# Kernel optimization log

Hardware: AMD Instinct MI355X
Metric: run time of the kernel (lower is better)

Reference implementation:

```python
import jax, jax.numpy as jnp
import numpy as np

NUM_ACTIVE = 2  # top-k active experts

def setup_inputs() -> dict:
    key = jax.random.key(0)
    ks = jax.random.split(key, 5)
    B, N, D, H, E = 8192, 16, 128, 384, 8
    x = jax.random.normal(ks[0], (B, N, D), dtype=jnp.float32)
    # xavier-ish scales for stability
    router_w = jax.random.normal(ks[1], (E, N * D), dtype=jnp.float32) * (1.0 / np.sqrt(N * D))
    w1 = jax.random.normal(ks[2], (E, N, D, H), dtype=jnp.float32) * (1.0 / np.sqrt(D))
    w_gate = jax.random.normal(ks[3], (E, N, D, H), dtype=jnp.float32) * (1.0 / np.sqrt(D))
    w2 = jax.random.normal(ks[4], (E, N, H, D), dtype=jnp.float32) * (1.0 / np.sqrt(H))
    return {"x": x, "router_w": router_w, "w1": w1, "w_gate": w_gate, "w2": w2}

def reference(x, router_w, w1, w_gate, w2):
    B, N, D = x.shape
    E = w1.shape[0]
    # shared router over flattened heads
    router_logits = x.reshape(B, N * D) @ router_w.T            # (B, E)
    topk_logits, topk_idx = jax.lax.top_k(router_logits, NUM_ACTIVE)
    topk_w = jax.nn.softmax(topk_logits, axis=-1)               # (B, K)
    # combined routing weight per (token, expert); zero if expert not selected
    onehot = jax.nn.one_hot(topk_idx, E, dtype=x.dtype)         # (B, K, E)
    w_tok_exp = jnp.einsum('bk,bke->be', topk_w, onehot)        # (B, E)
    out = jnp.zeros_like(x)
    # loop over fixed, small expert count; unselected tokens get weight 0
    for e in range(E):
        h1 = jnp.einsum('bnd,ndh->bnh', x, w1[e])
        gate = jnp.einsum('bnd,ndh->bnh', x, w_gate[e])
        h = h1 * jax.nn.silu(gate)                              # SwiGLU (dropout=0 / eval)
        out_e = jnp.einsum('bnh,nhd->bnd', h, w2[e])
        out = out + w_tok_exp[:, e][:, None, None] * out_e
    return out
```

## Files before the change

### kernel.cpp

```cpp
#include <hip/hip_runtime.h>

#define NTOK  8192
#define NHEAD 16
#define DDIM  128
#define HDIM  384
#define NEXP  8
#define TILE  128
#define ENTRIES 1280

typedef __attribute__((ext_vector_type(8))) short short8;
typedef __attribute__((ext_vector_type(4))) float f32x4;

#define SZ_WP    (128UL*12*24*512*2)
#define OFF_WP   0UL
#define OFF_ROUT (OFF_WP + SZ_WP)
#define OFF_CNT  (OFF_ROUT + 8192UL*16)
#define OFF_TAB  (OFF_CNT + 256)
#define OFF_LIST (OFF_TAB + 2UL*ENTRIES*16)
#define OFF_WL   (OFF_LIST + 2UL*8192*4)

struct Routing { int i0, i1; float w0, w1; };

__device__ __forceinline__ unsigned short f2bf(float f) {
  unsigned int u = __float_as_uint(f);
  u += 0x7fffu + ((u >> 16) & 1u);
  return (unsigned short)(u >> 16);
}

__device__ __forceinline__ void dma16(const unsigned short* g, char* l) {
  __builtin_amdgcn_global_load_lds(
      (const __attribute__((address_space(1))) unsigned int*)g,
      (__attribute__((address_space(3))) unsigned int*)l, 16, 0, 0);
}

__global__ __launch_bounds__(256) void convA_kernel(
    const float* __restrict__ w1, const float* __restrict__ wg,
    unsigned short* __restrict__ wP) {
  __shared__ float ls[32][388];
  const int kk = blockIdx.x;
  const int en = blockIdx.y;
  const int z  = blockIdx.z;
  const float* src = (z == 0 ? w1 : wg) + ((size_t)en * DDIM + kk * 32) * HDIM;
  const int tid = threadIdx.x;
  #pragma unroll
  for (int i = 0; i < 12; ++i) {
    int f4 = i * 256 + tid;
    int row = f4 / 96, c4 = f4 % 96;
    float4 v = reinterpret_cast<const float4*>(src + (size_t)row * HDIM)[c4];
    ls[row][c4*4+0] = v.x; ls[row][c4*4+1] = v.y;
    ls[row][c4*4+2] = v.z; ls[row][c4*4+3] = v.w;
  }
  __syncthreads();
  #pragma unroll
  for (int i = 0; i < 6; ++i) {
    int fid = i * 256 + tid;
    int ct = fid >> 6, lane = fid & 63;
    int r0 = (lane >> 4) * 8, c = ct * 16 + (lane & 15);
    unsigned short o[8];
    #pragma unroll
    for (int j = 0; j < 8; ++j) o[j] = f2bf(ls[r0 + j][c]);
    size_t off = (((size_t)en * 12 + (ct >> 1)) * 24 + (z * 8 + kk * 2 + (ct & 1))) * 512
               + (size_t)lane * 8;
    reinterpret_cast<uint4*>(wP + off)[0] =
        make_uint4((unsigned)o[0] | ((unsigned)o[1] << 16),
                   (unsigned)o[2] | ((unsigned)o[3] << 16),
                   (unsigned)o[4] | ((unsigned)o[5] << 16),
                   (unsigned)o[6] | ((unsigned)o[7] << 16));
  }
}

__global__ __launch_bounds__(256) void convB_kernel(
    const float* __restrict__ w2, unsigned short* __restrict__ wP) {
  __shared__ float ls[32][132];
  const int kk = blockIdx.x;
  const int en = blockIdx.y;
  const float* src = w2 + ((size_t)en * HDIM + kk * 32) * DDIM;
  const int tid = threadIdx.x;
  #pragma unroll
  for (int i = 0; i < 4; ++i) {
    int f4 = i * 256 + tid;
    int row = f4 >> 5, c4 = f4 & 31;
    float4 v = reinterpret_cast<const float4*>(src + (size_t)row * DDIM)[c4];
    ls[row][c4*4+0] = v.x; ls[row][c4*4+1] = v.y;
    ls[row][c4*4+2] = v.z; ls[row][c4*4+3] = v.w;
  }
  __syncthreads();
  #pragma unroll
  for (int i = 0; i < 2; ++i) {
    int fid = i * 256 + tid;
    int ct = fid >> 6, lane = fid & 63;
    int r0 = (lane >> 4) * 8, c = ct * 16 + (lane & 15);
    unsigned short o[8];
    #pragma unroll
    for (int j = 0; j < 8; ++j) o[j] = f2bf(ls[r0 + j][c]);
    size_t off = (((size_t)en * 12 + kk) * 24 + (16 + ct)) * 512 + (size_t)lane * 8;
    reinterpret_cast<uint4*>(wP + off)[0] =
        make_uint4((unsigned)o[0] | ((unsigned)o[1] << 16),
                   (unsigned)o[2] | ((unsigned)o[3] << 16),
                   (unsigned)o[4] | ((unsigned)o[5] << 16),
                   (unsigned)o[6] | ((unsigned)o[7] << 16));
  }
}

__global__ __launch_bounds__(256) void router_kernel(
    const float* __restrict__ x, const float* __restrict__ rw,
    Routing* __restrict__ routing) {
  const int lane = threadIdx.x & 63;
  const int wgid = blockIdx.x * 4 + (threadIdx.x >> 6);
  const int tok0 = wgid * 4;
  float acc[4][8];
  #pragma unroll
  for (int t = 0; t < 4; ++t)
    #pragma unroll
    for (int e = 0; e < 8; ++e) acc[t][e] = 0.f;
  const float4* xr = reinterpret_cast<const float4*>(x);
  const float4* wr = reinterpret_cast<const float4*>(rw);
  #pragma unroll
  for (int c = 0; c < 8; ++c) {
    float4 wv[8];
    #pragma unroll
    for (int e = 0; e < 8; ++e) wv[e] = wr[e * 512 + c * 64 + lane];
    #pragma unroll
    for (int t = 0; t < 4; ++t) {
      float4 xv = xr[(size_t)(tok0 + t) * 512 + c * 64 + lane];
      #pragma unroll
      for (int e = 0; e < 8; ++e)
        acc[t][e] += xv.x * wv[e].x + xv.y * wv[e].y + xv.z * wv[e].z + xv.w * wv[e].w;
    }
  }
  #pragma unroll
  for (int t = 0; t < 4; ++t)
    #pragma unroll
    for (int e = 0; e < 8; ++e) {
      acc[t][e] += __shfl_xor(acc[t][e], 1);
      acc[t][e] += __shfl_xor(acc[t][e], 2);
      acc[t][e] += __shfl_xor(acc[t][e], 4);
    }
  const int l3 = lane & 7;
  #pragma unroll
  for (int t = 0; t < 4; ++t) {
    float v0 = (l3 & 1) ? acc[t][1] : acc[t][0];
    float v1 = (l3 & 1) ? acc[t][3] : acc[t][2];
    float v2 = (l3 & 1) ? acc[t][5] : acc[t][4];
    float v3 = (l3 & 1) ? acc[t][7] : acc[t][6];
    float u0 = (l3 & 2) ? v1 : v0;
    float u1 = (l3 & 2) ? v3 : v2;
    float sel = (l3 & 4) ? u1 : u0;
    sel += __shfl_xor(sel, 8);
    sel += __shfl_xor(sel, 16);
    sel += __shfl_xor(sel, 32);
    float le[8];
    #pragma unroll
    for (int e = 0; e < 8; ++e) le[e] = __shfl(sel, e);
    if (lane == 0) {
      int tok = tok0 + t;
      int i0 = 0; float m0 = le[0];
      #pragma unroll
      for (int e = 1; e < 8; ++e) if (le[e] > m0) { m0 = le[e]; i0 = e; }
      int i1 = -1; float m1 = -3.4e38f;
      #pragma unroll
      for (int e = 0; e < 8; ++e) if (e != i0 && le[e] > m1) { m1 = le[e]; i1 = e; }
      float ed = __expf(m1 - m0);
      Routing r; r.i0 = i0; r.i1 = i1;
      r.w0 = 1.f / (1.f + ed); r.w1 = ed / (1.f + ed);
      routing[tok] = r;
    }
  }
}

__global__ __launch_bounds__(256) void count_kernel(
    const Routing* __restrict__ routing, int* __restrict__ cnt) {
  const int s = blockIdx.x >> 3, e = blockIdx.x & 7;
  const int tid = threadIdx.x;
  int c = 0;
  for (int t = tid; t < NTOK; t += 256) {
    Routing r = routing[t];
    c += ((s == 0 ? r.i0 : r.i1) == e);
  }
  c += __shfl_xor(c, 32); c += __shfl_xor(c, 16); c += __shfl_xor(c, 8);
  c += __shfl_xor(c, 4);  c += __shfl_xor(c, 2);  c += __shfl_xor(c, 1);
  __shared__ int wsum[4];
  if ((tid & 63) == 0) wsum[tid >> 6] = c;
  __syncthreads();
  if (tid == 0) cnt[blockIdx.x] = wsum[0] + wsum[1] + wsum[2] + wsum[3];
}

__global__ void build_kernel(const int* __restrict__ cnt, int* __restrict__ cur,
                             int4* __restrict__ table) {
  const int tid = threadIdx.x;
  for (int i = tid; i < 2 * ENTRIES; i += 256)
    table[i] = make_int4(0, 0, 0, 0);
  __syncthreads();
  if (tid < 16) {
    int s = tid >> 3, e = tid & 7;
    int base = 0;
    for (int k = 0; k < e; ++k) base += cnt[s * 8 + k];
    cur[tid] = base;
  }
  __syncthreads();
  if (tid < 16) {
    int s = tid >> 3, xcd = tid & 7;
    int j = 0;
    int base = 0;
    for (int e = 0; e < 8; ++e) {
      int c = cnt[s * 8 + e];
      #pragma unroll
      for (int nn = 0; nn < 2; ++nn) {
        int n = xcd + nn * 8;
        for (int t = 0; t < c; t += TILE) {
          int rc = c - t; if (rc > TILE) rc = TILE;
          table[s * ENTRIES + xcd + 8 * j] = make_int4(e, base + t, rc, n);
          ++j;
        }
      }
      base += c;
    }
  }
}

__global__ __launch_bounds__(256) void compact_kernel(
    const Routing* __restrict__ routing, const int* __restrict__ cur,
    int* __restrict__ list, float* __restrict__ wl) {
  const int s = blockIdx.x >> 3, e = blockIdx.x & 7;
  const int tid = threadIdx.x;
  __shared__ int ps[256];
  int myc = 0;
  for (int t = tid; t < NTOK; t += 256) {
    Routing r = routing[t];
    myc += ((s == 0 ? r.i0 : r.i1) == e);
  }
  ps[tid] = myc;
  __syncthreads();
  for (int off = 1; off < 256; off <<= 1) {
    int v = (tid >= off) ? ps[tid - off] : 0;
    __syncthreads();
    ps[tid] += v;
    __syncthreads();
  }
  int base = cur[blockIdx.x] + ps[tid] - myc;
  for (int t = tid; t < NTOK; t += 256) {
    Routing r = routing[t];
    int ei = (s == 0 ? r.i0 : r.i1);
    if (ei == e) {
      list[s * NTOK + base] = t;
      wl[s * NTOK + base] = (s == 0 ? r.w0 : r.w1);
      ++base;
    }
  }
}

__global__ __launch_bounds__(512, 4) void expert_kernel(
    const float* __restrict__ x,
    const unsigned short* __restrict__ wP,
    const int* __restrict__ list, const float* __restrict__ wl,
    const int4* __restrict__ table,
    float* __restrict__ out, const int slot)
{
  extern __shared__ char smem[];
  char* wb  = smem;
  char* pwb = smem + 49152;
  const int4 tb = table[slot * ENTRIES + blockIdx.x];
  const int e = tb.x, rbeg = tb.y, rcnt = tb.z, n = tb.w;
  if (rcnt == 0) return;
  const int* lst = list + slot * NTOK + rbeg;
  const float* wls = wl + slot * NTOK + rbeg;
  const int tid = threadIdx.x;
  const int wid = tid >> 6, lane = tid & 63;
  const int lr = lane & 15, lq = lane >> 4;
  const int tq = wid >> 1, ch = wid & 1;
  char* pq = pwb + tq * 2304;
  const f32x4 z4 = {0.f, 0.f, 0.f, 0.f};

  const unsigned short* wsrc = wP + (size_t)(e * NHEAD + n) * (12 * 24 * 512);

  short8 a[2][4];
  #pragma unroll
  for (int mi = 0; mi < 2; ++mi) {
    int row = tq * 32 + mi * 16 + lr;
    int ok = (row < rcnt);
    int tok = ok ? lst[row] : 0;
    const float* xp = x + ((size_t)tok * NHEAD + n) * DDIM;
    #pragma unroll
    for (int kk = 0; kk < 4; ++kk) {
      const float4* q = reinterpret_cast<const float4*>(xp + kk * 32 + lq * 8);
      float4 v0 = q[0], v1 = q[1];
      if (!ok) { v0 = make_float4(0,0,0,0); v1 = make_float4(0,0,0,0); }
      short8 t;
      t[0] = (short)f2bf(v0.x); t[1] = (short)f2bf(v0.y);
      t[2] = (short)f2bf(v0.z); t[3] = (short)f2bf(v0.w);
      t[4] = (short)f2bf(v1.x); t[5] = (short)f2bf(v1.y);
      t[6] = (short)f2bf(v1.z); t[7] = (short)f2bf(v1.w);
      a[mi][kk] = t;
    }
  }

  f32x4 acc[2][4];
  #pragma unroll
  for (int mi = 0; mi < 2; ++mi)
    #pragma unroll
    for (int ct = 0; ct < 4; ++ct) acc[mi][ct] = z4;

  #pragma unroll
  for (int i = 0; i < 3; ++i) {
    int seg = wid * 3 + i;
    dma16(wsrc + (size_t)seg * 512 + lane * 8, wb + seg * 1024);
  }

  #pragma unroll
  for (int c = 0; c < 12; ++c) {
    const int p = c & 1;
    char* wbp = wb + p * 24576;

    asm volatile("s_waitcnt lgkmcnt(0)" ::: "memory");
    __builtin_amdgcn_s_barrier();
    __builtin_amdgcn_sched_barrier(0);

    if (c < 11) {
      char* wbn = wb + (p ^ 1) * 24576;
      #pragma unroll
      for (int i = 0; i < 3; ++i) {
        int seg = wid * 3 + i;
        dma16(wsrc + ((size_t)(c + 1) * 24 + seg) * 512 + lane * 8, wbn + seg * 1024);
      }
      asm volatile("s_waitcnt vmcnt(3)" ::: "memory");
    } else {
      asm volatile("s_waitcnt vmcnt(0)" ::: "memory");
    }
    __builtin_amdgcn_s_barrier();
    __builtin_amdgcn_sched_barrier(0);

    {
      f32x4 ah[2], ag[2];
      ah[0] = ah[1] = z4; ag[0] = ag[1] = z4;
      #pragma unroll
      for (int kk = 0; kk < 4; ++kk) {
        short8 b1 = *reinterpret_cast<const short8*>(wbp + (kk * 2 + ch) * 1024 + lane * 16);
        short8 bg = *reinterpret_cast<const short8*>(wbp + 8192 + (kk * 2 + ch) * 1024 + lane * 16);
        #pragma unroll
        for (int mi = 0; mi < 2; ++mi) {
          ah[mi] = __builtin_amdgcn_mfma_f32_16x16x32_bf16(a[mi][kk], b1, ah[mi], 0, 0, 0);
          ag[mi] = __builtin_amdgcn_mfma_f32_16x16x32_bf16(a[mi][kk], bg, ag[mi], 0, 0, 0);
        }
      }
      #pragma unroll
      for (int mi = 0; mi < 2; ++mi)
        #pragma unroll
        for (int r = 0; r < 4; ++r) {
          float h1 = ah[mi][r], g = ag[mi][r];
          float val = h1 * g * __builtin_amdgcn_rcpf(1.f + __expf(-g));
          int rowq = mi * 16 + lq * 4 + r;
          int h = ch * 16 + lr;
          *reinterpret_cast<unsigned short*>(pq + rowq * 72 + h * 2) = f2bf(val);
        }
    }

    asm volatile("s_waitcnt lgkmcnt(0)" ::: "memory");
    __builtin_amdgcn_s_barrier();
    __builtin_amdgcn_sched_barrier(0);

    {
      short8 a2[2];
      #pragma unroll
      for (int mi = 0; mi < 2; ++mi)
        a2[mi] = *reinterpret_cast<const short8*>(pq + (mi * 16 + lr) * 72 + lq * 16);
      #pragma unroll
      for (int ct = 0; ct < 4; ++ct) {
        short8 b = *reinterpret_cast<const short8*>(wbp + (16 + ch * 4 + ct) * 1024 + lane * 16);
        acc[0][ct] = __builtin_amdgcn_mfma_f32_16x16x32_bf16(a2[0], b, acc[0][ct], 0, 0, 0);
        acc[1][ct] = __builtin_amdgcn_mfma_f32_16x16x32_bf16(a2[1], b, acc[1][ct], 0, 0, 0);
      }
    }
  }

  #pragma unroll
  for (int mi = 0; mi < 2; ++mi)
    #pragma unroll
    for (int r = 0; r < 4; ++r) {
      int row = tq * 32 + mi * 16 + lq * 4 + r;
      if (row < rcnt) {
        int tok = lst[row];
        float wt = wls[row];
        float* op = out + ((size_t)tok * NHEAD + n) * DDIM;
        #pragma unroll
        for (int ct = 0; ct < 4; ++ct) {
          int col = (ch * 4 + ct) * 16 + lr;
          float v = acc[mi][ct][r] * wt;
          if (slot == 0) op[col] = v;
          else          op[col] += v;
        }
      }
    }
}

extern "C" void kernel_launch(void* const* d_in, const int* in_sizes, int n_in,
                              void* d_out, int out_size, void* d_ws, size_t ws_size,
                              hipStream_t stream) {
  const float* x  = (const float*)d_in[0];
  const float* rw = (const float*)d_in[1];
  const float* w1 = (const float*)d_in[2];
  const float* wg = (const float*)d_in[3];
  const float* w2 = (const float*)d_in[4];
  float* out = (float*)d_out;
  char* ws = (char*)d_ws;

  unsigned short* wP = (unsigned short*)(ws + OFF_WP);
  Routing* routing = (Routing*)(ws + OFF_ROUT);
  int* cnt = (int*)(ws + OFF_CNT);
  int* cur = cnt + 16;
  int4* table = (int4*)(ws + OFF_TAB);
  int* list = (int*)(ws + OFF_LIST);
  float* wl = (float*)(ws + OFF_WL);

  convA_kernel<<<dim3(4, 128, 2), 256, 0, stream>>>(w1, wg, wP);
  convB_kernel<<<dim3(12, 128, 1), 256, 0, stream>>>(w2, wP);
  router_kernel<<<512, 256, 0, stream>>>(x, rw, routing);
  count_kernel<<<16, 256, 0, stream>>>(routing, cnt);
  build_kernel<<<1, 256, 0, stream>>>(cnt, cur, table);
  compact_kernel<<<16, 256, 0, stream>>>(routing, cur, list, wl);
  expert_kernel<<<ENTRIES, 512, 58368, stream>>>(
      x, wP, list, wl, table, out, 0);
  expert_kernel<<<ENTRIES, 512, 58368, stream>>>(
      x, wP, list, wl, table, out, 1);
}
```

Before: 274.0 us.

## Keep expert weights in registers and stream pre-gathered bf16 token tiles

```diff
diff --git a/kernel.cpp b/kernel.cpp
--- a/kernel.cpp
+++ b/kernel.cpp
@@ -5,8 +5,6 @@
 #define DDIM  128
 #define HDIM  384
 #define NEXP  8
-#define TILE  128
-#define ENTRIES 1280
 
 typedef __attribute__((ext_vector_type(8))) short short8;
 typedef __attribute__((ext_vector_type(4))) float f32x4;
@@ -15,9 +13,11 @@
 #define OFF_WP   0UL
 #define OFF_ROUT (OFF_WP + SZ_WP)
 #define OFF_CNT  (OFF_ROUT + 8192UL*16)
-#define OFF_TAB  (OFF_CNT + 256)
-#define OFF_LIST (OFF_TAB + 2UL*ENTRIES*16)
+#define OFF_LIST (OFF_CNT + 256)
 #define OFF_WL   (OFF_LIST + 2UL*8192*4)
+#define OFF_XG   (OFF_WL + 2UL*8192*4)
+#define XG_SLOT  (16UL*8192*128*2)
+#define XG_PAD   32768UL
 
 struct Routing { int i0, i1; float w0, w1; };
 
@@ -185,36 +185,13 @@
   if (tid == 0) cnt[blockIdx.x] = wsum[0] + wsum[1] + wsum[2] + wsum[3];
 }
 
-__global__ void build_kernel(const int* __restrict__ cnt, int* __restrict__ cur,
-                             int4* __restrict__ table) {
-  const int tid = threadIdx.x;
-  for (int i = tid; i < 2 * ENTRIES; i += 256)
-    table[i] = make_int4(0, 0, 0, 0);
-  __syncthreads();
+__global__ void build_kernel(const int* __restrict__ cnt, int* __restrict__ cur) {
+  int tid = threadIdx.x;
   if (tid < 16) {
     int s = tid >> 3, e = tid & 7;
-    int base = 0;
-    for (int k = 0; k < e; ++k) base += cnt[s * 8 + k];
-    cur[tid] = base;
-  }
-  __syncthreads();
-  if (tid < 16) {
-    int s = tid >> 3, xcd = tid & 7;
-    int j = 0;
-    int base = 0;
-    for (int e = 0; e < 8; ++e) {
-      int c = cnt[s * 8 + e];
-      #pragma unroll
-      for (int nn = 0; nn < 2; ++nn) {
-        int n = xcd + nn * 8;
-        for (int t = 0; t < c; t += TILE) {
-          int rc = c - t; if (rc > TILE) rc = TILE;
-          table[s * ENTRIES + xcd + 8 * j] = make_int4(e, base + t, rc, n);
-          ++j;
-        }
-      }
-      base += c;
-    }
+    int b = 0;
+    for (int k = 0; k < e; ++k) b += cnt[s * 8 + k];
+    cur[tid] = b;
   }
 }
 
@@ -249,147 +226,136 @@
   }
 }
 
-__global__ __launch_bounds__(512, 4) void expert_kernel(
-    const float* __restrict__ x,
+__global__ __launch_bounds__(256) void gather_kernel(
+    const float* __restrict__ x, const int* __restrict__ list,
+    unsigned short* __restrict__ xg, const int slot) {
+  const int tid = threadIdx.x;
+  const int n = tid >> 4, j = tid & 15;
+  for (int it = 0; it < 64; ++it) {
+    int pos = blockIdx.x * 64 + it;
+    int t = list[slot * NTOK + pos];
+    const float* src = x + ((size_t)t * NHEAD + n) * DDIM + j * 8;
+    float4 v0 = reinterpret_cast<const float4*>(src)[0];
+    float4 v1 = reinterpret_cast<const float4*>(src)[1];
+    uint4 w = make_uint4(
+        (unsigned)f2bf(v0.x) | ((unsigned)f2bf(v0.y) << 16),
+        (unsigned)f2bf(v0.z) | ((unsigned)f2bf(v0.w) << 16),
+        (unsigned)f2bf(v1.x) | ((unsigned)f2bf(v1.y) << 16),
+        (unsigned)f2bf(v1.z) | ((unsigned)f2bf(v1.w) << 16));
+    *reinterpret_cast<uint4*>(xg + ((size_t)n * NTOK + pos) * 128 + (size_t)((j ^ (pos & 7)) * 8)) = w;
+  }
+}
+
+__global__ __launch_bounds__(512, 2) void expert_kernel(
+    const unsigned short* __restrict__ xg,
     const unsigned short* __restrict__ wP,
     const int* __restrict__ list, const float* __restrict__ wl,
-    const int4* __restrict__ table,
+    const int* __restrict__ cnt,
     float* __restrict__ out, const int slot)
 {
   extern __shared__ char smem[];
-  char* wb  = smem;
-  char* pwb = smem + 49152;
-  const int4 tb = table[slot * ENTRIES + blockIdx.x];
-  const int e = tb.x, rbeg = tb.y, rcnt = tb.z, n = tb.w;
-  if (rcnt == 0) return;
-  const int* lst = list + slot * NTOK + rbeg;
-  const float* wls = wl + slot * NTOK + rbeg;
+  char* xls = smem;
+  char* P   = smem + 32768;
+  const int bid = blockIdx.x;
+  const int e = bid >> 5, n = (bid >> 1) & 15, kpar = bid & 1;
+  const int cntE  = cnt[slot * 8 + e];
+  const int ebase = cnt[16 + slot * 8 + e];
+  const int ntiles = (cntE + 127) >> 7;
+  if (kpar >= ntiles) return;
   const int tid = threadIdx.x;
   const int wid = tid >> 6, lane = tid & 63;
   const int lr = lane & 15, lq = lane >> 4;
-  const int tq = wid >> 1, ch = wid & 1;
-  char* pq = pwb + tq * 2304;
   const f32x4 z4 = {0.f, 0.f, 0.f, 0.f};
 
   const unsigned short* wsrc = wP + (size_t)(e * NHEAD + n) * (12 * 24 * 512);
-
-  short8 a[2][4];
-  #pragma unroll
-  for (int mi = 0; mi < 2; ++mi) {
-    int row = tq * 32 + mi * 16 + lr;
-    int ok = (row < rcnt);
-    int tok = ok ? lst[row] : 0;
-    const float* xp = x + ((size_t)tok * NHEAD + n) * DDIM;
+  short8 w1r[3][4], wgr[3][4], w2r[12];
+  #pragma unroll
+  for (int c = 0; c < 3; ++c) {
+    const int ctg = wid * 3 + c;
     #pragma unroll
     for (int kk = 0; kk < 4; ++kk) {
-      const float4* q = reinterpret_cast<const float4*>(xp + kk * 32 + lq * 8);
-      float4 v0 = q[0], v1 = q[1];
-      if (!ok) { v0 = make_float4(0,0,0,0); v1 = make_float4(0,0,0,0); }
-      short8 t;
-      t[0] = (short)f2bf(v0.x); t[1] = (short)f2bf(v0.y);
-      t[2] = (short)f2bf(v0.z); t[3] = (short)f2bf(v0.w);
-      t[4] = (short)f2bf(v1.x); t[5] = (short)f2bf(v1.y);
-      t[6] = (short)f2bf(v1.z); t[7] = (short)f2bf(v1.w);
-      a[mi][kk] = t;
-    }
-  }
-
-  f32x4 acc[2][4];
-  #pragma unroll
-  for (int mi = 0; mi < 2; ++mi)
-    #pragma unroll
-    for (int ct = 0; ct < 4; ++ct) acc[mi][ct] = z4;
-
-  #pragma unroll
-  for (int i = 0; i < 3; ++i) {
-    int seg = wid * 3 + i;
-    dma16(wsrc + (size_t)seg * 512 + lane * 8, wb + seg * 1024);
-  }
-
-  #pragma unroll
-  for (int c = 0; c < 12; ++c) {
-    const int p = c & 1;
-    char* wbp = wb + p * 24576;
-
+      size_t off = ((size_t)(ctg >> 1) * 24 + (kk * 2 + (ctg & 1))) * 512 + (size_t)lane * 8;
+      w1r[c][kk] = *reinterpret_cast<const short8*>(wsrc + off);
+      wgr[c][kk] = *reinterpret_cast<const short8*>(wsrc + off + 8 * 512);
+    }
+  }
+  #pragma unroll
+  for (int kk = 0; kk < 12; ++kk)
+    w2r[kk] = *reinterpret_cast<const short8*>(
+        wsrc + ((size_t)kk * 24 + 16 + wid) * 512 + (size_t)lane * 8);
+
+  const unsigned short* xbase = xg + ((size_t)n * NTOK + ebase) * 128;
+
+  {
+    const unsigned short* src = xbase + (size_t)kpar * 128 * 128 + wid * 2048;
+    #pragma unroll
+    for (int i = 0; i < 4; ++i)
+      dma16(src + i * 512 + lane * 8, xls + wid * 4096 + i * 1024);
+  }
+  asm volatile("s_waitcnt vmcnt(0)" ::: "memory");
+  __builtin_amdgcn_s_barrier();
+
+  for (int t = kpar; t < ntiles; t += 2) {
+    #pragma unroll 2
+    for (int mi = 0; mi < 8; ++mi) {
+      const int row = mi * 16 + lr;
+      const int key = ((ebase + row) & 7) << 4;
+      short8 a[4];
+      #pragma unroll
+      for (int kk = 0; kk < 4; ++kk)
+        a[kk] = *reinterpret_cast<const short8*>(xls + row * 256 + ((kk * 64 + lq * 16) ^ key));
+      #pragma unroll
+      for (int c = 0; c < 3; ++c) {
+        f32x4 ah = z4, ag = z4;
+        #pragma unroll
+        for (int kk = 0; kk < 4; ++kk) {
+          ah = __builtin_amdgcn_mfma_f32_16x16x32_bf16(a[kk], w1r[c][kk], ah, 0, 0, 0);
+          ag = __builtin_amdgcn_mfma_f32_16x16x32_bf16(a[kk], wgr[c][kk], ag, 0, 0, 0);
+        }
+        const int pcol = (wid * 3 + c) * 16 + lr;
+        #pragma unroll
+        for (int r = 0; r < 4; ++r) {
+          float h1 = ah[r], g = ag[r];
+          float val = h1 * g * __builtin_amdgcn_rcpf(1.f + __expf(-g));
+          int prow = mi * 16 + lq * 4 + r;
+          *reinterpret_cast<unsigned short*>(P + prow * 772 + pcol * 2) = f2bf(val);
+        }
+      }
+    }
     asm volatile("s_waitcnt lgkmcnt(0)" ::: "memory");
     __builtin_amdgcn_s_barrier();
-    __builtin_amdgcn_sched_barrier(0);
-
-    if (c < 11) {
-      char* wbn = wb + (p ^ 1) * 24576;
-      #pragma unroll
-      for (int i = 0; i < 3; ++i) {
-        int seg = wid * 3 + i;
-        dma16(wsrc + ((size_t)(c + 1) * 24 + seg) * 512 + lane * 8, wbn + seg * 1024);
+
+    if (t + 2 < ntiles) {
+      const unsigned short* src = xbase + (size_t)(t + 2) * 128 * 128 + wid * 2048;
+      #pragma unroll
+      for (int i = 0; i < 4; ++i)
+        dma16(src + i * 512 + lane * 8, xls + wid * 4096 + i * 1024);
+    }
+
+    #pragma unroll 2
+    for (int mi = 0; mi < 8; ++mi) {
+      f32x4 acc = z4;
+      #pragma unroll
+      for (int kk = 0; kk < 12; ++kk) {
+        short8 p = *reinterpret_cast<const short8*>(P + (mi * 16 + lr) * 772 + kk * 64 + lq * 16);
+        acc = __builtin_amdgcn_mfma_f32_16x16x32_bf16(p, w2r[kk], acc, 0, 0, 0);
       }
-      asm volatile("s_waitcnt vmcnt(3)" ::: "memory");
-    } else {
-      asm volatile("s_waitcnt vmcnt(0)" ::: "memory");
-    }
-    __builtin_amdgcn_s_barrier();
-    __builtin_amdgcn_sched_barrier(0);
-
-    {
-      f32x4 ah[2], ag[2];
-      ah[0] = ah[1] = z4; ag[0] = ag[1] = z4;
-      #pragma unroll
-      for (int kk = 0; kk < 4; ++kk) {
-        short8 b1 = *reinterpret_cast<const short8*>(wbp + (kk * 2 + ch) * 1024 + lane * 16);
-        short8 bg = *reinterpret_cast<const short8*>(wbp + 8192 + (kk * 2 + ch) * 1024 + lane * 16);
-        #pragma unroll
-        for (int mi = 0; mi < 2; ++mi) {
-          ah[mi] = __builtin_amdgcn_mfma_f32_16x16x32_bf16(a[mi][kk], b1, ah[mi], 0, 0, 0);
-          ag[mi] = __builtin_amdgcn_mfma_f32_16x16x32_bf16(a[mi][kk], bg, ag[mi], 0, 0, 0);
+      #pragma unroll
+      for (int r = 0; r < 4; ++r) {
+        int grow = t * 128 + mi * 16 + lq * 4 + r;
+        if (grow < cntE) {
+          int tok = list[slot * NTOK + ebase + grow];
+          float wt = wl[slot * NTOK + ebase + grow];
+          float* op = out + ((size_t)tok * NHEAD + n) * DDIM + wid * 16 + lr;
+          float v = acc[r] * wt;
+          if (slot == 0) *op = v;
+          else           *op += v;
         }
       }
-      #pragma unroll
-      for (int mi = 0; mi < 2; ++mi)
-        #pragma unroll
-        for (int r = 0; r < 4; ++r) {
-          float h1 = ah[mi][r], g = ag[mi][r];
-          float val = h1 * g * __builtin_amdgcn_rcpf(1.f + __expf(-g));
-          int rowq = mi * 16 + lq * 4 + r;
-          int h = ch * 16 + lr;
-          *reinterpret_cast<unsigned short*>(pq + rowq * 72 + h * 2) = f2bf(val);
-        }
-    }
-
-    asm volatile("s_waitcnt lgkmcnt(0)" ::: "memory");
+    }
+    asm volatile("s_waitcnt vmcnt(0)" ::: "memory");
     __builtin_amdgcn_s_barrier();
-    __builtin_amdgcn_sched_barrier(0);
-
-    {
-      short8 a2[2];
-      #pragma unroll
-      for (int mi = 0; mi < 2; ++mi)
-        a2[mi] = *reinterpret_cast<const short8*>(pq + (mi * 16 + lr) * 72 + lq * 16);
-      #pragma unroll
-      for (int ct = 0; ct < 4; ++ct) {
-        short8 b = *reinterpret_cast<const short8*>(wbp + (16 + ch * 4 + ct) * 1024 + lane * 16);
-        acc[0][ct] = __builtin_amdgcn_mfma_f32_16x16x32_bf16(a2[0], b, acc[0][ct], 0, 0, 0);
-        acc[1][ct] = __builtin_amdgcn_mfma_f32_16x16x32_bf16(a2[1], b, acc[1][ct], 0, 0, 0);
-      }
-    }
-  }
-
-  #pragma unroll
-  for (int mi = 0; mi < 2; ++mi)
-    #pragma unroll
-    for (int r = 0; r < 4; ++r) {
-      int row = tq * 32 + mi * 16 + lq * 4 + r;
-      if (row < rcnt) {
-        int tok = lst[row];
-        float wt = wls[row];
-        float* op = out + ((size_t)tok * NHEAD + n) * DDIM;
-        #pragma unroll
-        for (int ct = 0; ct < 4; ++ct) {
-          int col = (ch * 4 + ct) * 16 + lr;
-          float v = acc[mi][ct][r] * wt;
-          if (slot == 0) op[col] = v;
-          else          op[col] += v;
-        }
-      }
-    }
+  }
 }
 
 extern "C" void kernel_launch(void* const* d_in, const int* in_sizes, int n_in,
@@ -407,18 +373,30 @@
   Routing* routing = (Routing*)(ws + OFF_ROUT);
   int* cnt = (int*)(ws + OFF_CNT);
   int* cur = cnt + 16;
-  int4* table = (int4*)(ws + OFF_TAB);
   int* list = (int*)(ws + OFF_LIST);
   float* wl = (float*)(ws + OFF_WL);
+  unsigned short* xg0 = (unsigned short*)(ws + OFF_XG);
+
+  const size_t need2 = OFF_XG + 2 * XG_SLOT + XG_PAD;
+  const bool dual = (ws_size >= need2);
+  unsigned short* xg1 = dual ? (unsigned short*)(ws + OFF_XG + XG_SLOT) : xg0;
 
   convA_kernel<<<dim3(4, 128, 2), 256, 0, stream>>>(w1, wg, wP);
   convB_kernel<<<dim3(12, 128, 1), 256, 0, stream>>>(w2, wP);
   router_kernel<<<512, 256, 0, stream>>>(x, rw, routing);
   count_kernel<<<16, 256, 0, stream>>>(routing, cnt);
-  build_kernel<<<1, 256, 0, stream>>>(cnt, cur, table);
+  build_kernel<<<1, 64, 0, stream>>>(cnt, cur);
   compact_kernel<<<16, 256, 0, stream>>>(routing, cur, list, wl);
-  expert_kernel<<<ENTRIES, 512, 58368, stream>>>(
-      x, wP, list, wl, table, out, 0);
-  expert_kernel<<<ENTRIES, 512, 58368, stream>>>(
-      x, wP, list, wl, table, out, 1);
-}
+
+  if (dual) {
+    gather_kernel<<<128, 256, 0, stream>>>(x, list, xg0, 0);
+    gather_kernel<<<128, 256, 0, stream>>>(x, list, xg1, 1);
+    expert_kernel<<<256, 512, 131584, stream>>>(xg0, wP, list, wl, cnt, out, 0);
+    expert_kernel<<<256, 512, 131584, stream>>>(xg1, wP, list, wl, cnt, out, 1);
+  } else {
+    gather_kernel<<<128, 256, 0, stream>>>(x, list, xg0, 0);
+    expert_kernel<<<256, 512, 131584, stream>>>(xg0, wP, list, wl, cnt, out, 0);
+    gather_kernel<<<128, 256, 0, stream>>>(x, list, xg0, 1);
+    expert_kernel<<<256, 512, 131584, stream>>>(xg0, wP, list, wl, cnt, out, 1);
+  }
+}
```

Result: slower. 471.1 us (+71.9%).

## Pre-gather routed tokens into padded bf16 swizzled panels loaded via LDS DMA

Applied to the files above, without the earlier changes.

```diff
diff --git a/kernel.cpp b/kernel.cpp
--- a/kernel.cpp
+++ b/kernel.cpp
@@ -6,6 +6,7 @@
 #define HDIM  384
 #define NEXP  8
 #define TILE  128
+#define PADN  9216
 #define ENTRIES 1280
 
 typedef __attribute__((ext_vector_type(8))) short short8;
@@ -17,7 +18,10 @@
 #define OFF_CNT  (OFF_ROUT + 8192UL*16)
 #define OFF_TAB  (OFF_CNT + 256)
 #define OFF_LIST (OFF_TAB + 2UL*ENTRIES*16)
-#define OFF_WL   (OFF_LIST + 2UL*8192*4)
+#define OFF_POS  (OFF_LIST + 2UL*PADN*4)
+#define OFF_WL   (OFF_POS + 2UL*NTOK*4)
+#define OFF_XG   (OFF_WL + 2UL*PADN*4)
+#define XG_SLOT  (16UL*PADN*128*2)
 
 struct Routing { int i0, i1; float w0, w1; };
 
@@ -186,22 +190,23 @@
 }
 
 __global__ void build_kernel(const int* __restrict__ cnt, int* __restrict__ cur,
-                             int4* __restrict__ table) {
+                             int4* __restrict__ table, int* __restrict__ list) {
   const int tid = threadIdx.x;
   for (int i = tid; i < 2 * ENTRIES; i += 256)
     table[i] = make_int4(0, 0, 0, 0);
+  for (int i = tid; i < 2 * PADN; i += 256)
+    list[i] = -1;
   __syncthreads();
   if (tid < 16) {
     int s = tid >> 3, e = tid & 7;
-    int base = 0;
-    for (int k = 0; k < e; ++k) base += cnt[s * 8 + k];
-    cur[tid] = base;
+    int b = 0;
+    for (int k = 0; k < e; ++k) b += ((cnt[s * 8 + k] + 127) >> 7) << 7;
+    cur[tid] = b;
   }
   __syncthreads();
   if (tid < 16) {
     int s = tid >> 3, xcd = tid & 7;
-    int j = 0;
-    int base = 0;
+    int j = 0, ab = 0;
     for (int e = 0; e < 8; ++e) {
       int c = cnt[s * 8 + e];
       #pragma unroll
@@ -209,18 +214,18 @@
         int n = xcd + nn * 8;
         for (int t = 0; t < c; t += TILE) {
           int rc = c - t; if (rc > TILE) rc = TILE;
-          table[s * ENTRIES + xcd + 8 * j] = make_int4(e, base + t, rc, n);
+          table[s * ENTRIES + xcd + 8 * j] = make_int4(e, ab + t, rc, n);
           ++j;
         }
       }
-      base += c;
+      ab += ((c + 127) >> 7) << 7;
     }
   }
 }
 
 __global__ __launch_bounds__(256) void compact_kernel(
     const Routing* __restrict__ routing, const int* __restrict__ cur,
-    int* __restrict__ list, float* __restrict__ wl) {
+    int* __restrict__ list, float* __restrict__ wl, int* __restrict__ posmap) {
   const int s = blockIdx.x >> 3, e = blockIdx.x & 7;
   const int tid = threadIdx.x;
   __shared__ int ps[256];
@@ -242,15 +247,43 @@
     Routing r = routing[t];
     int ei = (s == 0 ? r.i0 : r.i1);
     if (ei == e) {
-      list[s * NTOK + base] = t;
-      wl[s * NTOK + base] = (s == 0 ? r.w0 : r.w1);
+      list[s * PADN + base] = t;
+      wl[s * PADN + base] = (s == 0 ? r.w0 : r.w1);
+      posmap[s * NTOK + t] = base;
       ++base;
     }
   }
 }
 
-__global__ __launch_bounds__(512, 4) void expert_kernel(
-    const float* __restrict__ x,
+__global__ __launch_bounds__(256) void gather_kernel(
+    const float* __restrict__ x, const int* __restrict__ posmap,
+    unsigned short* __restrict__ xg0, unsigned short* __restrict__ xg1,
+    const int mode) {
+  const int tid = threadIdx.x;
+  const int n = tid >> 4, j = tid & 15;
+  for (int it = 0; it < 32; ++it) {
+    int t = blockIdx.x * 32 + it;
+    const float* src = x + ((size_t)t * NHEAD + n) * DDIM + j * 8;
+    float4 v0 = reinterpret_cast<const float4*>(src)[0];
+    float4 v1 = reinterpret_cast<const float4*>(src)[1];
+    uint4 w = make_uint4(
+        (unsigned)f2bf(v0.x) | ((unsigned)f2bf(v0.y) << 16),
+        (unsigned)f2bf(v0.z) | ((unsigned)f2bf(v0.w) << 16),
+        (unsigned)f2bf(v1.x) | ((unsigned)f2bf(v1.y) << 16),
+        (unsigned)f2bf(v1.z) | ((unsigned)f2bf(v1.w) << 16));
+    if (mode != 2) {
+      int p0 = posmap[t];
+      *reinterpret_cast<uint4*>(xg0 + ((size_t)n * PADN + p0) * 128 + ((j ^ (p0 & 7)) * 8)) = w;
+    }
+    if (mode != 1) {
+      int p1 = posmap[NTOK + t];
+      *reinterpret_cast<uint4*>(xg1 + ((size_t)n * PADN + p1) * 128 + ((j ^ (p1 & 7)) * 8)) = w;
+    }
+  }
+}
+
+__global__ __launch_bounds__(512, 2) void expert_kernel(
+    const unsigned short* __restrict__ xg,
     const unsigned short* __restrict__ wP,
     const int* __restrict__ list, const float* __restrict__ wl,
     const int4* __restrict__ table,
@@ -262,8 +295,8 @@
   const int4 tb = table[slot * ENTRIES + blockIdx.x];
   const int e = tb.x, rbeg = tb.y, rcnt = tb.z, n = tb.w;
   if (rcnt == 0) return;
-  const int* lst = list + slot * NTOK + rbeg;
-  const float* wls = wl + slot * NTOK + rbeg;
+  const int* lst = list + slot * PADN + rbeg;
+  const float* wls = wl + slot * PADN + rbeg;
   const int tid = threadIdx.x;
   const int wid = tid >> 6, lane = tid & 63;
   const int lr = lane & 15, lq = lane >> 4;
@@ -272,27 +305,26 @@
   const f32x4 z4 = {0.f, 0.f, 0.f, 0.f};
 
   const unsigned short* wsrc = wP + (size_t)(e * NHEAD + n) * (12 * 24 * 512);
+  const unsigned short* xpan = xg + ((size_t)n * PADN + rbeg) * 128;
+
+  #pragma unroll
+  for (int i = 0; i < 4; ++i)
+    dma16(xpan + (size_t)wid * 2048 + i * 512 + lane * 8, wb + wid * 4096 + i * 1024);
+  asm volatile("s_waitcnt vmcnt(0)" ::: "memory");
+  __builtin_amdgcn_s_barrier();
 
   short8 a[2][4];
   #pragma unroll
   for (int mi = 0; mi < 2; ++mi) {
     int row = tq * 32 + mi * 16 + lr;
-    int ok = (row < rcnt);
-    int tok = ok ? lst[row] : 0;
-    const float* xp = x + ((size_t)tok * NHEAD + n) * DDIM;
-    #pragma unroll
-    for (int kk = 0; kk < 4; ++kk) {
-      const float4* q = reinterpret_cast<const float4*>(xp + kk * 32 + lq * 8);
-      float4 v0 = q[0], v1 = q[1];
-      if (!ok) { v0 = make_float4(0,0,0,0); v1 = make_float4(0,0,0,0); }
-      short8 t;
-      t[0] = (short)f2bf(v0.x); t[1] = (short)f2bf(v0.y);
-      t[2] = (short)f2bf(v0.z); t[3] = (short)f2bf(v0.w);
-      t[4] = (short)f2bf(v1.x); t[5] = (short)f2bf(v1.y);
-      t[6] = (short)f2bf(v1.z); t[7] = (short)f2bf(v1.w);
-      a[mi][kk] = t;
-    }
-  }
+    #pragma unroll
+    for (int kk = 0; kk < 4; ++kk)
+      a[mi][kk] = *reinterpret_cast<const short8*>(
+          wb + row * 256 + ((kk * 64 + lq * 16) ^ ((row & 7) << 4)));
+  }
+  asm volatile("s_waitcnt lgkmcnt(0)" ::: "memory");
+  __builtin_amdgcn_sched_barrier(0);
+  __builtin_amdgcn_s_barrier();
 
   f32x4 acc[2][4];
   #pragma unroll
@@ -409,16 +441,28 @@
   int* cur = cnt + 16;
   int4* table = (int4*)(ws + OFF_TAB);
   int* list = (int*)(ws + OFF_LIST);
+  int* posmap = (int*)(ws + OFF_POS);
   float* wl = (float*)(ws + OFF_WL);
+  unsigned short* xg0 = (unsigned short*)(ws + OFF_XG);
+
+  const bool dual = (ws_size >= OFF_XG + 2 * XG_SLOT);
+  unsigned short* xg1 = dual ? (unsigned short*)(ws + OFF_XG + XG_SLOT) : xg0;
 
   convA_kernel<<<dim3(4, 128, 2), 256, 0, stream>>>(w1, wg, wP);
   convB_kernel<<<dim3(12, 128, 1), 256, 0, stream>>>(w2, wP);
   router_kernel<<<512, 256, 0, stream>>>(x, rw, routing);
   count_kernel<<<16, 256, 0, stream>>>(routing, cnt);
-  build_kernel<<<1, 256, 0, stream>>>(cnt, cur, table);
-  compact_kernel<<<16, 256, 0, stream>>>(routing, cur, list, wl);
-  expert_kernel<<<ENTRIES, 512, 58368, stream>>>(
-      x, wP, list, wl, table, out, 0);
-  expert_kernel<<<ENTRIES, 512, 58368, stream>>>(
-      x, wP, list, wl, table, out, 1);
-}
+  build_kernel<<<1, 256, 0, stream>>>(cnt, cur, table, list);
+  compact_kernel<<<16, 256, 0, stream>>>(routing, cur, list, wl, posmap);
+
+  if (dual) {
+    gather_kernel<<<256, 256, 0, stream>>>(x, posmap, xg0, xg1, 0);
+    expert_kernel<<<ENTRIES, 512, 58368, stream>>>(xg0, wP, list, wl, table, out, 0);
+    expert_kernel<<<ENTRIES, 512, 58368, stream>>>(xg1, wP, list, wl, table, out, 1);
+  } else {
+    gather_kernel<<<256, 256, 0, stream>>>(x, posmap, xg0, xg0, 1);
+    expert_kernel<<<ENTRIES, 512, 58368, stream>>>(xg0, wP, list, wl, table, out, 0);
+    gather_kernel<<<256, 256, 0, stream>>>(x, posmap, xg0, xg0, 2);
+    expert_kernel<<<ENTRIES, 512, 58368, stream>>>(xg0, wP, list, wl, table, out, 1);
+  }
+}
```

After: 296.7 us. +8.3%, slower.

## Merge both top-k slot expert launches into one grid with temp buffer plus add

Applied to the files above, without the earlier changes.

```diff
diff --git a/kernel.cpp b/kernel.cpp
--- a/kernel.cpp
+++ b/kernel.cpp
@@ -18,6 +18,8 @@
 #define OFF_TAB  (OFF_CNT + 256)
 #define OFF_LIST (OFF_TAB + 2UL*ENTRIES*16)
 #define OFF_WL   (OFF_LIST + 2UL*8192*4)
+#define OFF_TMP  (OFF_WL + 2UL*8192*4)
+#define SZ_TMP   (8192UL*16*128*4)
 
 struct Routing { int i0, i1; float w0, w1; };
 
@@ -254,12 +256,17 @@
     const unsigned short* __restrict__ wP,
     const int* __restrict__ list, const float* __restrict__ wl,
     const int4* __restrict__ table,
-    float* __restrict__ out, const int slot)
+    float* __restrict__ dst0, float* __restrict__ dst1,
+    const int slotBase, const int rmwFlag)
 {
   extern __shared__ char smem[];
   char* wb  = smem;
   char* pwb = smem + 49152;
-  const int4 tb = table[slot * ENTRIES + blockIdx.x];
+  const int big = (blockIdx.x >= ENTRIES) ? 1 : 0;
+  const int slot = slotBase + big;
+  const int lid = blockIdx.x - big * ENTRIES;
+  float* const dstb = big ? dst1 : dst0;
+  const int4 tb = table[slot * ENTRIES + lid];
   const int e = tb.x, rbeg = tb.y, rcnt = tb.z, n = tb.w;
   if (rcnt == 0) return;
   const int* lst = list + slot * NTOK + rbeg;
@@ -380,16 +387,29 @@
       if (row < rcnt) {
         int tok = lst[row];
         float wt = wls[row];
-        float* op = out + ((size_t)tok * NHEAD + n) * DDIM;
+        float* op = dstb + ((size_t)tok * NHEAD + n) * DDIM;
         #pragma unroll
         for (int ct = 0; ct < 4; ++ct) {
           int col = (ch * 4 + ct) * 16 + lr;
           float v = acc[mi][ct][r] * wt;
-          if (slot == 0) op[col] = v;
-          else          op[col] += v;
+          if (rmwFlag) op[col] += v;
+          else         op[col] = v;
         }
       }
     }
+}
+
+__global__ __launch_bounds__(256) void add_kernel(
+    float4* __restrict__ out, const float4* __restrict__ tmp) {
+  const int i = blockIdx.x * 256 + threadIdx.x;
+  #pragma unroll
+  for (int k = 0; k < 8; ++k) {
+    int idx = i + k * (2048 * 256);
+    float4 a = out[idx];
+    float4 b = tmp[idx];
+    a.x += b.x; a.y += b.y; a.z += b.z; a.w += b.w;
+    out[idx] = a;
+  }
 }
 
 extern "C" void kernel_launch(void* const* d_in, const int* in_sizes, int n_in,
@@ -410,6 +430,7 @@
   int4* table = (int4*)(ws + OFF_TAB);
   int* list = (int*)(ws + OFF_LIST);
   float* wl = (float*)(ws + OFF_WL);
+  float* tmp = (float*)(ws + OFF_TMP);
 
   convA_kernel<<<dim3(4, 128, 2), 256, 0, stream>>>(w1, wg, wP);
   convB_kernel<<<dim3(12, 128, 1), 256, 0, stream>>>(w2, wP);
@@ -417,8 +438,16 @@
   count_kernel<<<16, 256, 0, stream>>>(routing, cnt);
   build_kernel<<<1, 256, 0, stream>>>(cnt, cur, table);
   compact_kernel<<<16, 256, 0, stream>>>(routing, cur, list, wl);
-  expert_kernel<<<ENTRIES, 512, 58368, stream>>>(
-      x, wP, list, wl, table, out, 0);
-  expert_kernel<<<ENTRIES, 512, 58368, stream>>>(
-      x, wP, list, wl, table, out, 1);
-}
+
+  if (ws_size >= OFF_TMP + SZ_TMP) {
+    expert_kernel<<<2 * ENTRIES, 512, 58368, stream>>>(
+        x, wP, list, wl, table, out, tmp, 0, 0);
+    add_kernel<<<2048, 256, 0, stream>>>(
+        reinterpret_cast<float4*>(out), reinterpret_cast<const float4*>(tmp));
+  } else {
+    expert_kernel<<<ENTRIES, 512, 58368, stream>>>(
+        x, wP, list, wl, table, out, out, 0, 0);
+    expert_kernel<<<ENTRIES, 512, 58368, stream>>>(
+        x, wP, list, wl, table, out, out, 1, 1);
+  }
+}
```

New measurement: 275.9 us. About the same (+0.7%).
